# Kernel optimization log

Hardware: AMD Instinct MI355X
Metric: run time of the kernel (lower is better)

## Reference

```python
import jax, jax.numpy as jnp
import numpy as np

D_MODEL = 1024
N_HEADS = 16
D_V = D_MODEL // N_HEADS  # 64; o_proj maps d_model -> d_v (quirk of the source)
B, S = 4, 2048


def setup_inputs() -> dict:
    key = jax.random.key(0)
    ks = jax.random.split(key, 5)
    scale = 1.0 / np.sqrt(D_MODEL)
    return {
        "in_features": jax.random.normal(ks[0], (B, S, D_MODEL), dtype=jnp.float32),
        "Wq": jax.random.normal(ks[1], (D_MODEL, D_MODEL), dtype=jnp.float32) * scale,
        "Wk": jax.random.normal(ks[2], (D_MODEL, D_MODEL), dtype=jnp.float32) * scale,
        "Wv": jax.random.normal(ks[3], (D_MODEL, D_MODEL), dtype=jnp.float32) * scale,
        "Wo": jax.random.normal(ks[4], (D_V, D_MODEL), dtype=jnp.float32) * scale,
    }


def reference(in_features, Wq, Wk, Wv, Wo):
    # Linear(in, out): y = x @ W^T, no bias. NOTE: source never splits heads;
    # attention runs single-head over the full d_model dims.
    Q = jnp.einsum('bsd,ed->bse', in_features, Wq)  # [B,S,D]
    K = jnp.einsum('bsd,ed->bse', in_features, Wk)
    V = jnp.einsum('bsd,ed->bse', in_features, Wv)

    scores = jnp.einsum('bqd,bkd->bqk', Q, K)       # [B,S,S]
    causal = jnp.tril(jnp.ones((S, S), dtype=bool))  # True = keep
    # source applies -inf mask BEFORE scaling (equivalent result)
    scores = jnp.where(causal[None, :, :], scores, -jnp.inf)
    scores = scores / jnp.sqrt(jnp.float32(D_MODEL))  # K.size(-1) == d_model
    attn = jax.nn.softmax(scores, axis=-1)
    ctx = jnp.einsum('bqk,bkd->bqd', attn, V)        # [B,S,D]
    return jnp.einsum('bsd,vd->bsv', ctx, Wo)        # [B,S,D_V]
```

## Files before the change

kernel.cpp:

```cpp
#include <hip/hip_runtime.h>
#include <math.h>

typedef unsigned short u16;
typedef unsigned int u32;
typedef __attribute__((ext_vector_type(8))) short short8;
typedef __attribute__((ext_vector_type(4))) short short4v;
typedef __attribute__((ext_vector_type(4))) float f32x4;

#define BB 4
#define SS 2048
#define DD 1024
#define DV 64
#define NYU 1152
#define BS (BB * SS)
#define SCALE (1.0f / 32.0f)

__device__ __forceinline__ u16 f2bf(float f) {
    u32 u = __builtin_bit_cast(u32, f);
    u32 r = u + 0x7fffu + ((u >> 16) & 1u);
    return (u16)(r >> 16);
}
__device__ __forceinline__ float bf2f(u16 b) {
    return __builtin_bit_cast(float, (u32)b << 16);
}
__device__ __forceinline__ void storeC(float* p, float v) { *p = v; }
__device__ __forceinline__ void storeC(u16* p, float v) { *p = f2bf(v); }

__global__ __launch_bounds__(256) void prep(const float* __restrict__ x,
                                            const float* __restrict__ Wq,
                                            const float* __restrict__ Wk,
                                            const float* __restrict__ Wo,
                                            const float* __restrict__ Wv,
                                            u16* __restrict__ x16,
                                            u16* __restrict__ Wqt,
                                            u16* __restrict__ Wkt,
                                            float* __restrict__ wpart,
                                            float* __restrict__ out,
                                            float* __restrict__ Lacc) {
    __shared__ float smem[64 * 128];
    const int b = blockIdx.x;
    const int tid = threadIdx.x;
    if (b < 8192) {
        int i = b * 256 + tid;
        f32x4 v = ((const f32x4*)x)[i];
        short4v o;
        o.x = (short)f2bf(v.x); o.y = (short)f2bf(v.y);
        o.z = (short)f2bf(v.z); o.w = (short)f2bf(v.w);
        ((short4v*)x16)[i] = o;
    } else if (b < 8704) {
        const int bb = b - 8192;
        const float* src = (bb >> 8) ? Wk : Wq;
        u16* dst = (bb >> 8) ? Wkt : Wqt;
        const int rem = bb & 255;
        const int e0 = (rem >> 4) * 64, d0 = (rem & 15) * 64;
        u16* t = (u16*)smem;
        const int g = tid >> 6, lane = tid & 63;
        for (int r = g; r < 64; r += 4)
            t[r * 72 + lane] = f2bf(src[(size_t)(e0 + r) * DD + d0 + lane]);
        __syncthreads();
        for (int r = g; r < 64; r += 4)
            dst[(size_t)(d0 + r) * DD + e0 + lane] = t[lane * 72 + r];
    } else if (b < 8768) {
        const int bb = b - 8704;
        const int echunk = (bb & 7) * 128;
        const int kc = bb >> 3, kbase = kc * 128;
        for (int idx = tid; idx < 64 * 128; idx += 256)
            smem[idx] = Wo[(size_t)(idx >> 7) * DD + kbase + (idx & 127)];
        __syncthreads();
        const int eo = echunk + (tid & 31) * 4;
        const int ob = (tid >> 5) * 8;
        float acc[8][4] = {};
        for (int k = 0; k < 128; ++k) {
            f32x4 wv = *(const f32x4*)&Wv[(size_t)(kbase + k) * DD + eo];
#pragma unroll
            for (int oi = 0; oi < 8; ++oi) {
                float s = smem[(ob + oi) * 128 + k];
                acc[oi][0] += s * wv.x; acc[oi][1] += s * wv.y;
                acc[oi][2] += s * wv.z; acc[oi][3] += s * wv.w;
            }
        }
#pragma unroll
        for (int oi = 0; oi < 8; ++oi)
            *(f32x4*)&wpart[((size_t)kc * 64 + ob + oi) * DD + eo] =
                (f32x4){acc[oi][0], acc[oi][1], acc[oi][2], acc[oi][3]};
    } else if (b < 9280) {
        int i = (b - 8768) * 256 + tid;
        ((f32x4*)out)[i] = (f32x4){0.f, 0.f, 0.f, 0.f};
    } else {
        int i = (b - 9280) * 256 + tid;
        ((f32x4*)Lacc)[i] = (f32x4){0.f, 0.f, 0.f, 0.f};
    }
}

__global__ __launch_bounds__(256) void reduce_all(const float* __restrict__ Gpart,
                                                  const float* __restrict__ wpart,
                                                  u16* __restrict__ Wall2) {
    const int bx = blockIdx.x;
    const int e0 = threadIdx.x * 4;
    f32x4 s = (f32x4){0.f, 0.f, 0.f, 0.f};
    if (bx < 1024) {
#pragma unroll
        for (int kc = 0; kc < 4; ++kc)
            s += *(const f32x4*)&Gpart[(size_t)kc * DD * DD + (size_t)bx * DD + e0];
    } else {
#pragma unroll
        for (int kc = 0; kc < 8; ++kc)
            s += *(const f32x4*)&wpart[((size_t)kc * 64 + bx - 1024) * DD + e0];
    }
    short4v ov;
    ov.x = (short)f2bf(s.x); ov.y = (short)f2bf(s.y);
    ov.z = (short)f2bf(s.z); ov.w = (short)f2bf(s.w);
    *(short4v*)&Wall2[(size_t)bx * DD + e0] = ov;
}

template <int TM, int TN, int WM, int WN, typename OutT, int MODE>
__global__ __launch_bounds__(WM * WN * 64) void gemm_nt_mfma(
    const u16* __restrict__ A, const u16* __restrict__ B, OutT* __restrict__ C,
    int lda, int ldb, int ldc, int K, long sA, long sB, long sC,
    u16* __restrict__ Utp) {
    constexpr int NW = WM * WN;
    constexpr int CA = TM / 16;
    constexpr int CB = TN / 16;

    const int z = blockIdx.z;
    A += (size_t)z * sA;
    B += (size_t)z * sB;
    C += (size_t)z * sC;
    int m0, n0;
    if constexpr (MODE == 3) {
        const int b = blockIdx.x;
        const int r = b & 7, q = b >> 3;
        m0 = (r * 8 + q / 9) * TM;
        n0 = (q % 9) * TN;
    } else {
        m0 = blockIdx.y * TM;
        n0 = blockIdx.x * TN;
    }

    __shared__ u16 As[TM * 32];
    __shared__ u16 Bs[TN * 32];

    const int tid = threadIdx.x;
    const int w = tid >> 6, lane = tid & 63;
    const int wm = w / WN, wn = w % WN;
    const int lrow = lane >> 2;
    const int lcol = (lane & 3) * 8;
    const int m16 = lane & 15;
    const int kh = (lane >> 4) * 8;

    f32x4 acc[4][4];
#pragma unroll
    for (int i = 0; i < 4; ++i)
#pragma unroll
        for (int j = 0; j < 4; ++j) acc[i][j] = (f32x4){0.f, 0.f, 0.f, 0.f};

    for (int k0 = 0; k0 < K; k0 += 32) {
        for (int c = w; c < CA; c += NW) {
            const u16* g = A + (size_t)(m0 + c * 16 + lrow) * lda + k0 + lcol;
            __builtin_amdgcn_global_load_lds(
                (const __attribute__((address_space(1))) void*)g,
                (__attribute__((address_space(3))) void*)(&As[c * 512]), 16, 0, 0);
        }
        for (int c = w; c < CB; c += NW) {
            const u16* g = B + (size_t)(n0 + c * 16 + lrow) * ldb + k0 + lcol;
            __builtin_amdgcn_global_load_lds(
                (const __attribute__((address_space(1))) void*)g,
                (__attribute__((address_space(3))) void*)(&Bs[c * 512]), 16, 0, 0);
        }
        __syncthreads();

        short8 a[4], b[4];
#pragma unroll
        for (int i = 0; i < 4; ++i)
            a[i] = *(const short8*)&As[(wm * 64 + i * 16 + m16) * 32 + kh];
#pragma unroll
        for (int j = 0; j < 4; ++j)
            b[j] = *(const short8*)&Bs[(wn * 64 + j * 16 + m16) * 32 + kh];
#pragma unroll
        for (int i = 0; i < 4; ++i)
#pragma unroll
            for (int j = 0; j < 4; ++j)
                acc[i][j] = __builtin_amdgcn_mfma_f32_16x16x32_bf16(a[i], b[j], acc[i][j], 0, 0, 0);
        __syncthreads();
    }

    const int crow0 = m0 + wm * 64 + (lane >> 4) * 4;
    const int ccol0 = n0 + wn * 64 + m16;
#pragma unroll
    for (int i = 0; i < 4; ++i)
#pragma unroll
        for (int j = 0; j < 4; ++j)
#pragma unroll
            for (int r = 0; r < 4; ++r) {
                const float v = acc[i][j][r];
                storeC(&C[(size_t)(crow0 + i * 16 + r) * ldc + ccol0 + j * 16], v);
                if constexpr (MODE == 3) {
                    if (n0 == 1024 && wn == 0)
                        Utp[(size_t)(ccol0 + j * 16 - 1024) * BS + crow0 + i * 16 + r] = f2bf(v);
                }
            }
}

__global__ __launch_bounds__(256) void scores_pv(const u16* __restrict__ YU,
                                                 const u16* __restrict__ x16,
                                                 const u16* __restrict__ Ut,
                                                 float* __restrict__ out,
                                                 float* __restrict__ Lacc) {
    const int b = blockIdx.x;
    const int r8 = b & 7;
    const int z = r8 >> 1;
    const int t = 2 * (b >> 3) + (r8 & 1);
    int y = (int)((sqrtf(8.f * t + 1.f) - 1.f) * 0.5f);
    while ((y + 1) * (y + 2) / 2 <= t) ++y;
    while (y * (y + 1) / 2 > t) --y;
    const int m0 = y * 128;
    const int n0 = (t - y * (y + 1) / 2) * 128;

    const u16* A = YU + (size_t)z * SS * NYU;
    const u16* B = x16 + (size_t)z * SS * DD;

    __shared__ union ShU {
        struct { u16 As[128 * 32]; u16 Bs[128 * 32]; } s;
        u16 Ps[128 * 136];
    } sh;

    const int tid = threadIdx.x;
    const int w = tid >> 6, lane = tid & 63;
    const int wm = w >> 1, wn = w & 1;
    const int lrow = lane >> 2;
    const int lcol = (lane & 3) * 8;
    const int m16 = lane & 15;
    const int kh = (lane >> 4) * 8;

    f32x4 acc[4][4];
#pragma unroll
    for (int i = 0; i < 4; ++i)
#pragma unroll
        for (int j = 0; j < 4; ++j) acc[i][j] = (f32x4){0.f, 0.f, 0.f, 0.f};

    for (int k0 = 0; k0 < DD; k0 += 32) {
        for (int c = w; c < 8; c += 4) {
            const u16* g = A + (size_t)(m0 + c * 16 + lrow) * NYU + k0 + lcol;
            __builtin_amdgcn_global_load_lds(
                (const __attribute__((address_space(1))) void*)g,
                (__attribute__((address_space(3))) void*)(&sh.s.As[c * 512]), 16, 0, 0);
        }
        for (int c = w; c < 8; c += 4) {
            const u16* g = B + (size_t)(n0 + c * 16 + lrow) * DD + k0 + lcol;
            __builtin_amdgcn_global_load_lds(
                (const __attribute__((address_space(1))) void*)g,
                (__attribute__((address_space(3))) void*)(&sh.s.Bs[c * 512]), 16, 0, 0);
        }
        __syncthreads();

        short8 a[4], bb[4];
#pragma unroll
        for (int i = 0; i < 4; ++i)
            a[i] = *(const short8*)&sh.s.As[(wm * 64 + i * 16 + m16) * 32 + kh];
#pragma unroll
        for (int j = 0; j < 4; ++j)
            bb[j] = *(const short8*)&sh.s.Bs[(wn * 64 + j * 16 + m16) * 32 + kh];
#pragma unroll
        for (int i = 0; i < 4; ++i)
#pragma unroll
            for (int j = 0; j < 4; ++j)
                acc[i][j] = __builtin_amdgcn_mfma_f32_16x16x32_bf16(a[i], bb[j], acc[i][j], 0, 0, 0);
        __syncthreads();
    }

    const int rl0 = wm * 64 + (lane >> 4) * 4;
    const int cl0 = wn * 64 + m16;
#pragma unroll
    for (int i = 0; i < 4; ++i)
#pragma unroll
        for (int j = 0; j < 4; ++j)
#pragma unroll
            for (int r = 0; r < 4; ++r) {
                const int rl = rl0 + i * 16 + r;
                const int cl = cl0 + j * 16;
                float p = __expf(acc[i][j][r] * SCALE);
                sh.Ps[rl * 136 + cl] = (n0 + cl <= m0 + rl) ? f2bf(p) : (u16)0;
            }
    __syncthreads();

    short8 ones8;
#pragma unroll
    for (int e = 0; e < 8; ++e) ones8[e] = (short)0x3F80;

    const u16* Utz = Ut + (size_t)z * SS + n0;
    f32x4 accO[2][4], accL[2];
#pragma unroll
    for (int i = 0; i < 2; ++i) {
        accL[i] = (f32x4){0.f, 0.f, 0.f, 0.f};
#pragma unroll
        for (int j = 0; j < 4; ++j) accO[i][j] = (f32x4){0.f, 0.f, 0.f, 0.f};
    }
#pragma unroll
    for (int ks = 0; ks < 4; ++ks) {
        const int k0 = ks * 32;
        short8 a[2], bb[4];
#pragma unroll
        for (int i = 0; i < 2; ++i)
            a[i] = *(const short8*)&sh.Ps[(w * 32 + i * 16 + m16) * 136 + k0 + kh];
#pragma unroll
        for (int j = 0; j < 4; ++j)
            bb[j] = *(const short8*)&Utz[(size_t)(j * 16 + m16) * BS + k0 + kh];
#pragma unroll
        for (int i = 0; i < 2; ++i) {
#pragma unroll
            for (int j = 0; j < 4; ++j)
                accO[i][j] = __builtin_amdgcn_mfma_f32_16x16x32_bf16(a[i], bb[j], accO[i][j], 0, 0, 0);
            accL[i] = __builtin_amdgcn_mfma_f32_16x16x32_bf16(a[i], ones8, accL[i], 0, 0, 0);
        }
    }

    float* Oz = out + (size_t)z * SS * DV;
    float* Lz = Lacc + (size_t)z * SS;
    const int wrow = m0 + w * 32 + (lane >> 4) * 4;
#pragma unroll
    for (int i = 0; i < 2; ++i) {
#pragma unroll
        for (int j = 0; j < 4; ++j)
#pragma unroll
            for (int r = 0; r < 4; ++r)
                atomicAdd(&Oz[(size_t)(wrow + i * 16 + r) * DV + j * 16 + m16],
                          accO[i][j][r]);
        if (m16 == 0)
#pragma unroll
            for (int r = 0; r < 4; ++r)
                atomicAdd(&Lz[wrow + i * 16 + r], accL[i][r]);
    }
}

__global__ __launch_bounds__(256) void normalize(float* __restrict__ out,
                                                 const float* __restrict__ Lacc) {
    int i = blockIdx.x * 256 + threadIdx.x;
    f32x4 v = ((f32x4*)out)[i];
    const float inv = 1.f / Lacc[(i * 4) >> 6];
    v.x *= inv; v.y *= inv; v.z *= inv; v.w *= inv;
    ((f32x4*)out)[i] = v;
}

extern "C" void kernel_launch(void* const* d_in, const int* in_sizes, int n_in,
                              void* d_out, int out_size, void* d_ws, size_t ws_size,
                              hipStream_t stream) {
    const float* x  = (const float*)d_in[0];
    const float* Wq = (const float*)d_in[1];
    const float* Wk = (const float*)d_in[2];
    const float* Wv = (const float*)d_in[3];
    const float* Wo = (const float*)d_in[4];
    float* out = (float*)d_out;

    u16* x16   = (u16*)d_ws;
    u16* Wqt16 = x16 + (size_t)BB * SS * DD;
    u16* Wkt16 = Wqt16 + (size_t)DD * DD;
    u16* Wall2 = Wkt16 + (size_t)DD * DD;
    u16* YU    = Wall2 + (size_t)NYU * DD;
    u16* Ut    = YU + (size_t)BB * SS * NYU;
    float* wpart = (float*)(Ut + (size_t)DV * BS);
    float* Lacc  = wpart + (size_t)8 * 64 * DD;
    float* Gpart = (float*)YU;

    prep<<<dim3(9288), 256, 0, stream>>>(x, Wq, Wk, Wo, Wv, x16, Wqt16, Wkt16,
                                         wpart, out, Lacc);

    gemm_nt_mfma<128, 128, 2, 2, float, 0><<<dim3(8, 8, 4), 256, 0, stream>>>(
        Wkt16, Wqt16, Gpart, DD, DD, DD, 256, 256, 256, (long)DD * DD, nullptr);

    reduce_all<<<dim3(1088), 256, 0, stream>>>(Gpart, wpart, Wall2);

    gemm_nt_mfma<128, 128, 2, 2, u16, 3><<<dim3(576), 256, 0, stream>>>(
        x16, Wall2, YU, DD, DD, NYU, DD, 0, 0, 0, Ut);

    scores_pv<<<dim3(544), 256, 0, stream>>>(YU, x16, Ut, out, Lacc);

    normalize<<<dim3(out_size / 4 / 256), 256, 0, stream>>>(out, Lacc);
}
```

Baseline: 204.4 us.

## Split K across two warp groups in YU GEMM and scores kernel

The YU projection GEMM and the scores/PV kernel now run 512 threads per block. Two groups of four warps each handle one half of the K=1024 reduction in separate LDS buffers, then combine their partial accumulators through shared-memory scratch in two phases. This doubles the waves per tile to hide load latency, since grids of 544–576 blocks give few waves per CU. In exchange it adds an LDS reduction with extra barriers, doubles LDS use per block, and may lower occupancy. The PV stage is also reworked so each of the 8 warps handles 16 rows.

```diff
diff --git a/kernel.cpp b/kernel.cpp
--- a/kernel.cpp
+++ b/kernel.cpp
@@ -113,36 +113,21 @@
     *(short4v*)&Wall2[(size_t)bx * DD + e0] = ov;
 }
 
-template <int TM, int TN, int WM, int WN, typename OutT, int MODE>
-__global__ __launch_bounds__(WM * WN * 64) void gemm_nt_mfma(
-    const u16* __restrict__ A, const u16* __restrict__ B, OutT* __restrict__ C,
-    int lda, int ldb, int ldc, int K, long sA, long sB, long sC,
-    u16* __restrict__ Utp) {
-    constexpr int NW = WM * WN;
-    constexpr int CA = TM / 16;
-    constexpr int CB = TN / 16;
-
+__global__ __launch_bounds__(256) void gemm_nt_small(
+    const u16* __restrict__ A, const u16* __restrict__ B, float* __restrict__ C,
+    int lda, int ldb, int ldc, int K, long sA, long sB, long sC) {
     const int z = blockIdx.z;
     A += (size_t)z * sA;
     B += (size_t)z * sB;
     C += (size_t)z * sC;
-    int m0, n0;
-    if constexpr (MODE == 3) {
-        const int b = blockIdx.x;
-        const int r = b & 7, q = b >> 3;
-        m0 = (r * 8 + q / 9) * TM;
-        n0 = (q % 9) * TN;
-    } else {
-        m0 = blockIdx.y * TM;
-        n0 = blockIdx.x * TN;
-    }
-
-    __shared__ u16 As[TM * 32];
-    __shared__ u16 Bs[TN * 32];
+    const int m0 = blockIdx.y * 128, n0 = blockIdx.x * 128;
+
+    __shared__ u16 As[128 * 32];
+    __shared__ u16 Bs[128 * 32];
 
     const int tid = threadIdx.x;
     const int w = tid >> 6, lane = tid & 63;
-    const int wm = w / WN, wn = w % WN;
+    const int wm = w >> 1, wn = w & 1;
     const int lrow = lane >> 2;
     const int lcol = (lane & 3) * 8;
     const int m16 = lane & 15;
@@ -155,20 +140,19 @@
         for (int j = 0; j < 4; ++j) acc[i][j] = (f32x4){0.f, 0.f, 0.f, 0.f};
 
     for (int k0 = 0; k0 < K; k0 += 32) {
-        for (int c = w; c < CA; c += NW) {
+        for (int c = w; c < 8; c += 4) {
             const u16* g = A + (size_t)(m0 + c * 16 + lrow) * lda + k0 + lcol;
             __builtin_amdgcn_global_load_lds(
                 (const __attribute__((address_space(1))) void*)g,
                 (__attribute__((address_space(3))) void*)(&As[c * 512]), 16, 0, 0);
         }
-        for (int c = w; c < CB; c += NW) {
+        for (int c = w; c < 8; c += 4) {
             const u16* g = B + (size_t)(n0 + c * 16 + lrow) * ldb + k0 + lcol;
             __builtin_amdgcn_global_load_lds(
                 (const __attribute__((address_space(1))) void*)g,
                 (__attribute__((address_space(3))) void*)(&Bs[c * 512]), 16, 0, 0);
         }
         __syncthreads();
-
         short8 a[4], b[4];
 #pragma unroll
         for (int i = 0; i < 4; ++i)
@@ -183,7 +167,6 @@
                 acc[i][j] = __builtin_amdgcn_mfma_f32_16x16x32_bf16(a[i], b[j], acc[i][j], 0, 0, 0);
         __syncthreads();
     }
-
     const int crow0 = m0 + wm * 64 + (lane >> 4) * 4;
     const int ccol0 = n0 + wn * 64 + m16;
 #pragma unroll
@@ -191,17 +174,114 @@
 #pragma unroll
         for (int j = 0; j < 4; ++j)
 #pragma unroll
-            for (int r = 0; r < 4; ++r) {
-                const float v = acc[i][j][r];
-                storeC(&C[(size_t)(crow0 + i * 16 + r) * ldc + ccol0 + j * 16], v);
-                if constexpr (MODE == 3) {
+            for (int r = 0; r < 4; ++r)
+                C[(size_t)(crow0 + i * 16 + r) * ldc + ccol0 + j * 16] = acc[i][j][r];
+}
+
+__global__ __launch_bounds__(512) void yu_8w(const u16* __restrict__ A,
+                                             const u16* __restrict__ B,
+                                             u16* __restrict__ C,
+                                             u16* __restrict__ Utp) {
+    const int b = blockIdx.x;
+    const int r = b & 7, q = b >> 3;
+    const int m0 = (r * 8 + q / 9) * 128;
+    const int n0 = (q % 9) * 128;
+
+    __shared__ union ShU {
+        struct { u16 As[2][128 * 32]; u16 Bs[2][128 * 32]; } s;
+        float scr[64 * 132];
+    } sh;
+
+    const int tid = threadIdx.x;
+    const int w = tid >> 6, lane = tid & 63;
+    const int g = w >> 2, wg = w & 3;
+    const int wm = wg >> 1, wn = wg & 1;
+    const int lrow = lane >> 2;
+    const int lcol = (lane & 3) * 8;
+    const int m16 = lane & 15;
+    const int kh = (lane >> 4) * 8;
+    const int q4 = (lane >> 4) * 4;
+
+    f32x4 acc[4][4];
+#pragma unroll
+    for (int i = 0; i < 4; ++i)
+#pragma unroll
+        for (int j = 0; j < 4; ++j) acc[i][j] = (f32x4){0.f, 0.f, 0.f, 0.f};
+
+    const int kbase = g * 512;
+    for (int k0 = 0; k0 < 512; k0 += 32) {
+        for (int c = wg; c < 8; c += 4) {
+            const u16* gp = A + (size_t)(m0 + c * 16 + lrow) * DD + kbase + k0 + lcol;
+            __builtin_amdgcn_global_load_lds(
+                (const __attribute__((address_space(1))) void*)gp,
+                (__attribute__((address_space(3))) void*)(&sh.s.As[g][c * 512]), 16, 0, 0);
+        }
+        for (int c = wg; c < 8; c += 4) {
+            const u16* gp = B + (size_t)(n0 + c * 16 + lrow) * DD + kbase + k0 + lcol;
+            __builtin_amdgcn_global_load_lds(
+                (const __attribute__((address_space(1))) void*)gp,
+                (__attribute__((address_space(3))) void*)(&sh.s.Bs[g][c * 512]), 16, 0, 0);
+        }
+        __syncthreads();
+        short8 a[4], bb[4];
+#pragma unroll
+        for (int i = 0; i < 4; ++i)
+            a[i] = *(const short8*)&sh.s.As[g][(wm * 64 + i * 16 + m16) * 32 + kh];
+#pragma unroll
+        for (int j = 0; j < 4; ++j)
+            bb[j] = *(const short8*)&sh.s.Bs[g][(wn * 64 + j * 16 + m16) * 32 + kh];
+#pragma unroll
+        for (int i = 0; i < 4; ++i)
+#pragma unroll
+            for (int j = 0; j < 4; ++j)
+                acc[i][j] = __builtin_amdgcn_mfma_f32_16x16x32_bf16(a[i], bb[j], acc[i][j], 0, 0, 0);
+        __syncthreads();
+    }
+
+#pragma unroll
+    for (int ph = 0; ph < 2; ++ph) {
+        if (g == 1 && wm == ph) {
+#pragma unroll
+            for (int i = 0; i < 4; ++i)
+#pragma unroll
+                for (int j = 0; j < 4; ++j)
+#pragma unroll
+                    for (int rr = 0; rr < 4; ++rr)
+                        sh.scr[(i * 16 + q4 + rr) * 132 + wn * 64 + j * 16 + m16] = acc[i][j][rr];
+        }
+        __syncthreads();
+        if (g == 0 && wm == ph) {
+#pragma unroll
+            for (int i = 0; i < 4; ++i)
+#pragma unroll
+                for (int j = 0; j < 4; ++j)
+#pragma unroll
+                    for (int rr = 0; rr < 4; ++rr)
+                        acc[i][j][rr] += sh.scr[(i * 16 + q4 + rr) * 132 + wn * 64 + j * 16 + m16];
+        }
+        __syncthreads();
+    }
+
+    if (g == 0) {
+        const int crow0 = m0 + wm * 64 + q4;
+        const int ccol0 = n0 + wn * 64 + m16;
+#pragma unroll
+        for (int i = 0; i < 4; ++i)
+#pragma unroll
+            for (int j = 0; j < 4; ++j)
+#pragma unroll
+                for (int rr = 0; rr < 4; ++rr) {
+                    const float v = acc[i][j][rr];
+                    const int row = crow0 + i * 16 + rr;
+                    const int col = ccol0 + j * 16;
+                    C[(size_t)row * NYU + col] = f2bf(v);
                     if (n0 == 1024 && wn == 0)
-                        Utp[(size_t)(ccol0 + j * 16 - 1024) * BS + crow0 + i * 16 + r] = f2bf(v);
+                        Utp[(size_t)(col - 1024) * BS + row] = f2bf(v);
                 }
-            }
-}
-
-__global__ __launch_bounds__(256) void scores_pv(const u16* __restrict__ YU,
+    }
+}
+
+__global__ __launch_bounds__(512) void scores_pv(const u16* __restrict__ YU,
                                                  const u16* __restrict__ x16,
                                                  const u16* __restrict__ Ut,
                                                  float* __restrict__ out,
@@ -220,17 +300,20 @@
     const u16* B = x16 + (size_t)z * SS * DD;
 
     __shared__ union ShU {
-        struct { u16 As[128 * 32]; u16 Bs[128 * 32]; } s;
+        struct { u16 As[2][128 * 32]; u16 Bs[2][128 * 32]; } s;
         u16 Ps[128 * 136];
+        float scr[64 * 132];
     } sh;
 
     const int tid = threadIdx.x;
     const int w = tid >> 6, lane = tid & 63;
-    const int wm = w >> 1, wn = w & 1;
+    const int g = w >> 2, wg = w & 3;
+    const int wm = wg >> 1, wn = wg & 1;
     const int lrow = lane >> 2;
     const int lcol = (lane & 3) * 8;
     const int m16 = lane & 15;
     const int kh = (lane >> 4) * 8;
+    const int q4 = (lane >> 4) * 4;
 
     f32x4 acc[4][4];
 #pragma unroll
@@ -238,28 +321,28 @@
 #pragma unroll
         for (int j = 0; j < 4; ++j) acc[i][j] = (f32x4){0.f, 0.f, 0.f, 0.f};
 
-    for (int k0 = 0; k0 < DD; k0 += 32) {
-        for (int c = w; c < 8; c += 4) {
-            const u16* g = A + (size_t)(m0 + c * 16 + lrow) * NYU + k0 + lcol;
-            __builtin_amdgcn_global_load_lds(
-                (const __attribute__((address_space(1))) void*)g,
-                (__attribute__((address_space(3))) void*)(&sh.s.As[c * 512]), 16, 0, 0);
-        }
-        for (int c = w; c < 8; c += 4) {
-            const u16* g = B + (size_t)(n0 + c * 16 + lrow) * DD + k0 + lcol;
-            __builtin_amdgcn_global_load_lds(
-                (const __attribute__((address_space(1))) void*)g,
-                (__attribute__((address_space(3))) void*)(&sh.s.Bs[c * 512]), 16, 0, 0);
-        }
-        __syncthreads();
-
+    const int kbase = g * 512;
+    for (int k0 = 0; k0 < 512; k0 += 32) {
+        for (int c = wg; c < 8; c += 4) {
+            const u16* gp = A + (size_t)(m0 + c * 16 + lrow) * NYU + kbase + k0 + lcol;
+            __builtin_amdgcn_global_load_lds(
+                (const __attribute__((address_space(1))) void*)gp,
+                (__attribute__((address_space(3))) void*)(&sh.s.As[g][c * 512]), 16, 0, 0);
+        }
+        for (int c = wg; c < 8; c += 4) {
+            const u16* gp = B + (size_t)(n0 + c * 16 + lrow) * DD + kbase + k0 + lcol;
+            __builtin_amdgcn_global_load_lds(
+                (const __attribute__((address_space(1))) void*)gp,
+                (__attribute__((address_space(3))) void*)(&sh.s.Bs[g][c * 512]), 16, 0, 0);
+        }
+        __syncthreads();
         short8 a[4], bb[4];
 #pragma unroll
         for (int i = 0; i < 4; ++i)
-            a[i] = *(const short8*)&sh.s.As[(wm * 64 + i * 16 + m16) * 32 + kh];
-#pragma unroll
-        for (int j = 0; j < 4; ++j)
-            bb[j] = *(const short8*)&sh.s.Bs[(wn * 64 + j * 16 + m16) * 32 + kh];
+            a[i] = *(const short8*)&sh.s.As[g][(wm * 64 + i * 16 + m16) * 32 + kh];
+#pragma unroll
+        for (int j = 0; j < 4; ++j)
+            bb[j] = *(const short8*)&sh.s.Bs[g][(wn * 64 + j * 16 + m16) * 32 + kh];
 #pragma unroll
         for (int i = 0; i < 4; ++i)
 #pragma unroll
@@ -268,19 +351,45 @@
         __syncthreads();
     }
 
-    const int rl0 = wm * 64 + (lane >> 4) * 4;
-    const int cl0 = wn * 64 + m16;
-#pragma unroll
-    for (int i = 0; i < 4; ++i)
-#pragma unroll
-        for (int j = 0; j < 4; ++j)
-#pragma unroll
-            for (int r = 0; r < 4; ++r) {
-                const int rl = rl0 + i * 16 + r;
-                const int cl = cl0 + j * 16;
-                float p = __expf(acc[i][j][r] * SCALE);
-                sh.Ps[rl * 136 + cl] = (n0 + cl <= m0 + rl) ? f2bf(p) : (u16)0;
-            }
+#pragma unroll
+    for (int ph = 0; ph < 2; ++ph) {
+        if (g == 1 && wm == ph) {
+#pragma unroll
+            for (int i = 0; i < 4; ++i)
+#pragma unroll
+                for (int j = 0; j < 4; ++j)
+#pragma unroll
+                    for (int rr = 0; rr < 4; ++rr)
+                        sh.scr[(i * 16 + q4 + rr) * 132 + wn * 64 + j * 16 + m16] = acc[i][j][rr];
+        }
+        __syncthreads();
+        if (g == 0 && wm == ph) {
+#pragma unroll
+            for (int i = 0; i < 4; ++i)
+#pragma unroll
+                for (int j = 0; j < 4; ++j)
+#pragma unroll
+                    for (int rr = 0; rr < 4; ++rr)
+                        acc[i][j][rr] += sh.scr[(i * 16 + q4 + rr) * 132 + wn * 64 + j * 16 + m16];
+        }
+        __syncthreads();
+    }
+
+    if (g == 0) {
+        const int rl0 = wm * 64 + q4;
+        const int cl0 = wn * 64 + m16;
+#pragma unroll
+        for (int i = 0; i < 4; ++i)
+#pragma unroll
+            for (int j = 0; j < 4; ++j)
+#pragma unroll
+                for (int rr = 0; rr < 4; ++rr) {
+                    const int rl = rl0 + i * 16 + rr;
+                    const int cl = cl0 + j * 16;
+                    float p = __expf(acc[i][j][rr] * SCALE);
+                    sh.Ps[rl * 136 + cl] = (n0 + cl <= m0 + rl) ? f2bf(p) : (u16)0;
+                }
+    }
     __syncthreads();
 
     short8 ones8;
@@ -288,48 +397,36 @@
     for (int e = 0; e < 8; ++e) ones8[e] = (short)0x3F80;
 
     const u16* Utz = Ut + (size_t)z * SS + n0;
-    f32x4 accO[2][4], accL[2];
-#pragma unroll
-    for (int i = 0; i < 2; ++i) {
-        accL[i] = (f32x4){0.f, 0.f, 0.f, 0.f};
-#pragma unroll
-        for (int j = 0; j < 4; ++j) accO[i][j] = (f32x4){0.f, 0.f, 0.f, 0.f};
-    }
+    f32x4 accO[4], accL;
+    accL = (f32x4){0.f, 0.f, 0.f, 0.f};
+#pragma unroll
+    for (int j = 0; j < 4; ++j) accO[j] = (f32x4){0.f, 0.f, 0.f, 0.f};
 #pragma unroll
     for (int ks = 0; ks < 4; ++ks) {
         const int k0 = ks * 32;
-        short8 a[2], bb[4];
-#pragma unroll
-        for (int i = 0; i < 2; ++i)
-            a[i] = *(const short8*)&sh.Ps[(w * 32 + i * 16 + m16) * 136 + k0 + kh];
+        short8 a = *(const short8*)&sh.Ps[(w * 16 + m16) * 136 + k0 + kh];
+        short8 bb[4];
 #pragma unroll
         for (int j = 0; j < 4; ++j)
             bb[j] = *(const short8*)&Utz[(size_t)(j * 16 + m16) * BS + k0 + kh];
 #pragma unroll
-        for (int i = 0; i < 2; ++i) {
-#pragma unroll
-            for (int j = 0; j < 4; ++j)
-                accO[i][j] = __builtin_amdgcn_mfma_f32_16x16x32_bf16(a[i], bb[j], accO[i][j], 0, 0, 0);
-            accL[i] = __builtin_amdgcn_mfma_f32_16x16x32_bf16(a[i], ones8, accL[i], 0, 0, 0);
-        }
+        for (int j = 0; j < 4; ++j)
+            accO[j] = __builtin_amdgcn_mfma_f32_16x16x32_bf16(a, bb[j], accO[j], 0, 0, 0);
+        accL = __builtin_amdgcn_mfma_f32_16x16x32_bf16(a, ones8, accL, 0, 0, 0);
     }
 
     float* Oz = out + (size_t)z * SS * DV;
     float* Lz = Lacc + (size_t)z * SS;
-    const int wrow = m0 + w * 32 + (lane >> 4) * 4;
-#pragma unroll
-    for (int i = 0; i < 2; ++i) {
-#pragma unroll
-        for (int j = 0; j < 4; ++j)
-#pragma unroll
-            for (int r = 0; r < 4; ++r)
-                atomicAdd(&Oz[(size_t)(wrow + i * 16 + r) * DV + j * 16 + m16],
-                          accO[i][j][r]);
-        if (m16 == 0)
-#pragma unroll
-            for (int r = 0; r < 4; ++r)
-                atomicAdd(&Lz[wrow + i * 16 + r], accL[i][r]);
-    }
+    const int wrow = m0 + w * 16 + q4;
+#pragma unroll
+    for (int j = 0; j < 4; ++j)
+#pragma unroll
+        for (int rr = 0; rr < 4; ++rr)
+            atomicAdd(&Oz[(size_t)(wrow + rr) * DV + j * 16 + m16], accO[j][rr]);
+    if (m16 == 0)
+#pragma unroll
+        for (int rr = 0; rr < 4; ++rr)
+            atomicAdd(&Lz[wrow + rr], accL[rr]);
 }
 
 __global__ __launch_bounds__(256) void normalize(float* __restrict__ out,
@@ -364,15 +461,14 @@
     prep<<<dim3(9288), 256, 0, stream>>>(x, Wq, Wk, Wo, Wv, x16, Wqt16, Wkt16,
                                          wpart, out, Lacc);
 
-    gemm_nt_mfma<128, 128, 2, 2, float, 0><<<dim3(8, 8, 4), 256, 0, stream>>>(
-        Wkt16, Wqt16, Gpart, DD, DD, DD, 256, 256, 256, (long)DD * DD, nullptr);
+    gemm_nt_small<<<dim3(8, 8, 4), 256, 0, stream>>>(
+        Wkt16, Wqt16, Gpart, DD, DD, DD, 256, 256, 256, (long)DD * DD);
 
     reduce_all<<<dim3(1088), 256, 0, stream>>>(Gpart, wpart, Wall2);
 
-    gemm_nt_mfma<128, 128, 2, 2, u16, 3><<<dim3(576), 256, 0, stream>>>(
-        x16, Wall2, YU, DD, DD, NYU, DD, 0, 0, 0, Ut);
-
-    scores_pv<<<dim3(544), 256, 0, stream>>>(YU, x16, Ut, out, Lacc);
+    yu_8w<<<dim3(576), 512, 0, stream>>>(x16, Wall2, YU, Ut);
+
+    scores_pv<<<dim3(544), 512, 0, stream>>>(YU, x16, Ut, out, Lacc);
 
     normalize<<<dim3(out_size / 4 / 256), 256, 0, stream>>>(out, Lacc);
 }
```

Measured after the change: 297.0 us. +45.3%, slower.
